# Performance work log

Measured on AMD Instinct MI355X. Metric: run time of the kernel, lower is better.

Reference implementation:

```python
import jax, jax.numpy as jnp
import numpy as np

H = 128  # hidden_dim
F = 64   # node_feat_dim


def setup_inputs() -> dict:
    key = jax.random.key(0)
    ks = jax.random.split(key, 24)
    N, E, NR, NT = 50000, 400000, 20000, 20000
    inp = {
        "mol_x": jax.random.normal(ks[0], (N, F), jnp.float32),
        "pos": jax.random.normal(ks[1], (N, 3), jnp.float32),
        "reaction_x": jax.random.normal(ks[2], (NR, F), jnp.float32),
        "target_x": jax.random.normal(ks[3], (NT, F), jnp.float32),
        "edge_index": jax.random.randint(ks[4], (2, E), 0, N, jnp.int32),
    }
    def lin(k, fan_in, fan_out):
        s = 1.0 / np.sqrt(fan_in)
        kw, kb = jax.random.split(k)
        W = jax.random.uniform(kw, (fan_in, fan_out), jnp.float32, -s, s)
        b = jax.random.uniform(kb, (fan_out,), jnp.float32, -s, s)
        return W, b
    inp["W_node"], inp["b_node"] = lin(ks[5], F, H)
    inp["W_att1"], inp["b_att1"] = lin(ks[6], 2 * H + 3, H)
    inp["W_att2"], inp["b_att2"] = lin(ks[7], H, 1)
    inp["W_upd"], inp["b_upd"] = lin(ks[8], H, H)
    inp["Wy1"], inp["by1"] = lin(ks[9], H, 64)
    inp["Wy2"], inp["by2"] = lin(ks[10], 64, 1)
    inp["Wa1"], inp["ba1"] = lin(ks[11], H, 64)
    inp["Wa2"], inp["ba2"] = lin(ks[12], 64, 1)
    return inp


def reference(mol_x, pos, reaction_x, target_x, edge_index,
              W_node, b_node, W_att1, b_att1, W_att2, b_att2,
              W_upd, b_upd, Wy1, by1, Wy2, by2, Wa1, ba1, Wa2, ba2):
    N = mol_x.shape[0]
    # node encoder
    h = mol_x @ W_node + b_node                      # [N, H]
    src, dst = edge_index[0], edge_index[1]          # PyG: x_j = source, x_i = target
    x_j = h[src]                                      # [E, H]
    x_i = h[dst]                                      # [E, H]
    dist = pos[dst] - pos[src]                        # [E, 3]
    cat = jnp.concatenate([x_i, x_j, dist], axis=1)   # [E, 2H+3]
    s = jax.nn.relu(cat @ W_att1 + b_att1) @ W_att2 + b_att2  # [E, 1]
    att = jax.nn.softmax(s, axis=0)                   # global softmax over edges (dim=0)
    msg = x_j * att                                   # [E, H]
    aggr = jax.ops.segment_sum(msg, dst, num_segments=N)  # scatter-add -> [N, H]
    mol_feats = aggr @ W_upd + b_upd                  # [N, H]
    # heads on reaction / target graphs
    rh = reaction_x @ W_node + b_node
    th = target_x @ W_node + b_node
    pred_yield = (jax.nn.relu(rh @ Wy1 + by1) @ Wy2 + by2).squeeze(-1)
    pred_activity = (jax.nn.relu(th @ Wa1 + ba1) @ Wa2 + ba2).squeeze(-1)
    return pred_yield, pred_activity, mol_feats
```

## Files before the change

### kernel.cpp

```cpp
#include <hip/hip_runtime.h>
#include <hip/hip_bf16.h>

typedef unsigned short ushort_t;
typedef __attribute__((ext_vector_type(8))) short s16x8;
typedef __attribute__((ext_vector_type(4))) float f32x4;

__device__ inline unsigned short f2bf(float x) {
    unsigned u = __float_as_uint(x);
    return (unsigned short)((u + 0x7FFFu + ((u >> 16) & 1u)) >> 16);
}
__device__ inline float bflo(unsigned u) { return __uint_as_float(u << 16); }
__device__ inline float bfhi(unsigned u) { return __uint_as_float(u & 0xffff0000u); }

__device__ inline void pack_one(const float* __restrict__ W, int K, int N,
                                ushort_t* __restrict__ dst, int g) {
    int KT = K / 32;
    int nt = g / (KT * 64);
    int rem = g % (KT * 64);
    int kt = rem / 64, lane = rem % 64;
    int n = nt * 16 + (lane & 15);
    int kbase = kt * 32 + ((lane >> 4) << 3);
    ushort_t tmp[8];
#pragma unroll
    for (int j = 0; j < 8; ++j) tmp[j] = f2bf(W[(size_t)(kbase + j) * N + n]);
    uint4 pk;
    pk.x = tmp[0] | ((unsigned)tmp[1] << 16);
    pk.y = tmp[2] | ((unsigned)tmp[3] << 16);
    pk.z = tmp[4] | ((unsigned)tmp[5] << 16);
    pk.w = tmp[6] | ((unsigned)tmp[7] << 16);
    *(uint4*)&dst[(size_t)g * 8] = pk;
}

__global__ void convert_w(const float* __restrict__ Wn, const float* __restrict__ W1,
                          const float* __restrict__ Wu, const float* __restrict__ Wy1,
                          const float* __restrict__ Wa1,
                          ushort_t* __restrict__ Wnb, ushort_t* __restrict__ W1tb,
                          ushort_t* __restrict__ W1mb, ushort_t* __restrict__ Wub,
                          ushort_t* __restrict__ Wy1b, ushort_t* __restrict__ Wa1b,
                          int* __restrict__ counts, int N) {
    int t = blockIdx.x * 256 + threadIdx.x;
    if (t < 1024)       pack_one(Wn, 64, 128, Wnb, t);
    else if (t < 3072)  pack_one(W1, 128, 128, W1tb, t - 1024);
    else if (t < 5120)  pack_one(W1 + 128 * 128, 128, 128, W1mb, t - 3072);
    else if (t < 7168)  pack_one(Wu, 128, 128, Wub, t - 5120);
    else if (t < 8192)  pack_one(Wy1, 128, 64, Wy1b, t - 7168);
    else if (t < 9216)  pack_one(Wa1, 128, 64, Wa1b, t - 8192);
    if (t < N) counts[t] = 0;
}

__global__ void encode_pq(const float* __restrict__ x, const ushort_t* __restrict__ Wnb,
                          const float* __restrict__ bn, const ushort_t* __restrict__ W1tb,
                          const ushort_t* __restrict__ W1mb, const float* __restrict__ b1,
                          ushort_t* __restrict__ hb, ushort_t* __restrict__ P,
                          ushort_t* __restrict__ Q, const int* __restrict__ dst,
                          int* __restrict__ counts, int nrows, int E) {
    __shared__ ushort_t ldsH[4 * 16 * 136];
    int t = threadIdx.x;
    for (int e = blockIdx.x * 256 + t; e < E; e += gridDim.x * 256)
        atomicAdd(&counts[dst[e]], 1);
    int w = t >> 6, lane = t & 63;
    int c = lane & 15, q = lane >> 4;
    int r0 = blockIdx.x * 64 + w * 16;
    int rowA = r0 + c; if (rowA >= nrows) rowA = nrows - 1;
    ushort_t* myH = &ldsH[w * 16 * 136];

    s16x8 xa[2];
#pragma unroll
    for (int kt = 0; kt < 2; ++kt) {
        const float* xp = &x[(size_t)rowA * 64 + kt * 32 + q * 8];
        float4 v0 = *(const float4*)xp;
        float4 v1 = *(const float4*)(xp + 4);
        s16x8 a;
        a[0] = (short)f2bf(v0.x); a[1] = (short)f2bf(v0.y);
        a[2] = (short)f2bf(v0.z); a[3] = (short)f2bf(v0.w);
        a[4] = (short)f2bf(v1.x); a[5] = (short)f2bf(v1.y);
        a[6] = (short)f2bf(v1.z); a[7] = (short)f2bf(v1.w);
        xa[kt] = a;
    }
#pragma unroll
    for (int nt = 0; nt < 8; ++nt) {
        f32x4 acc = {0.f, 0.f, 0.f, 0.f};
#pragma unroll
        for (int kt = 0; kt < 2; ++kt) {
            s16x8 b = *(const s16x8*)&Wnb[((nt * 2 + kt) * 64 + lane) * 8];
            acc = __builtin_amdgcn_mfma_f32_16x16x32_bf16(xa[kt], b, acc, 0, 0, 0);
        }
        float bi = bn[nt * 16 + c];
#pragma unroll
        for (int r = 0; r < 4; ++r) {
            int row = r0 + q * 4 + r;
            ushort_t hv = f2bf(acc[r] + bi);
            myH[(q * 4 + r) * 136 + nt * 16 + c] = hv;
            if (row < nrows) hb[(size_t)row * 128 + nt * 16 + c] = hv;
        }
    }
    __syncthreads();
    s16x8 ha[4];
#pragma unroll
    for (int kt = 0; kt < 4; ++kt)
        ha[kt] = *(const s16x8*)&myH[c * 136 + kt * 32 + q * 8];
#pragma unroll
    for (int nt = 0; nt < 8; ++nt) {
        f32x4 pa = {0.f, 0.f, 0.f, 0.f}, qa = pa;
#pragma unroll
        for (int kt = 0; kt < 4; ++kt) {
            s16x8 bp = *(const s16x8*)&W1tb[((nt * 4 + kt) * 64 + lane) * 8];
            s16x8 bq = *(const s16x8*)&W1mb[((nt * 4 + kt) * 64 + lane) * 8];
            pa = __builtin_amdgcn_mfma_f32_16x16x32_bf16(ha[kt], bp, pa, 0, 0, 0);
            qa = __builtin_amdgcn_mfma_f32_16x16x32_bf16(ha[kt], bq, qa, 0, 0, 0);
        }
        float bi = b1[nt * 16 + c];
#pragma unroll
        for (int r = 0; r < 4; ++r) {
            int row = r0 + q * 4 + r;
            if (row < nrows) {
                P[(size_t)row * 128 + nt * 16 + c] = f2bf(pa[r] + bi);
                Q[(size_t)row * 128 + nt * 16 + c] = f2bf(qa[r]);
            }
        }
    }
}

__global__ void scan1(const int* __restrict__ counts, int* __restrict__ offs,
                      int* __restrict__ partials, int N) {
    __shared__ int sm[256];
    int i = blockIdx.x * 256 + threadIdx.x;
    int v = (i < N) ? counts[i] : 0;
    sm[threadIdx.x] = v; __syncthreads();
    for (int off = 1; off < 256; off <<= 1) {
        int add = (threadIdx.x >= off) ? sm[threadIdx.x - off] : 0;
        __syncthreads();
        sm[threadIdx.x] += add;
        __syncthreads();
    }
    if (i < N) offs[i] = sm[threadIdx.x] - v;
    if (threadIdx.x == 255) partials[blockIdx.x] = sm[255];
}

__global__ void scan_add(int* __restrict__ offs, int* __restrict__ cursor,
                         const int* __restrict__ partials, int nb, int N) {
    __shared__ int sm[256];
    int t = threadIdx.x;
    sm[t] = (t < nb && t < blockIdx.x) ? partials[t] : 0;
    __syncthreads();
    for (int off = 128; off > 0; off >>= 1) {
        if (t < off) sm[t] += sm[t + off];
        __syncthreads();
    }
    int basev = sm[0];
    int i = blockIdx.x * 256 + t;
    if (i < N) {
        int v = offs[i] + basev;
        offs[i] = v;
        cursor[i] = v;
    }
}

__global__ __launch_bounds__(256, 4)
void edge_score(const ushort_t* __restrict__ P, const ushort_t* __restrict__ Q,
                const float* __restrict__ pos, const int* __restrict__ src,
                const int* __restrict__ dst, const float* __restrict__ W1b,
                const float* __restrict__ W2, const float* __restrict__ b2,
                int* __restrict__ cursor, int2* __restrict__ csr,
                float* __restrict__ redm, float* __restrict__ rede, int E) {
    __shared__ float wsh[512];
    __shared__ float smm[4], sme[4];
    int t = threadIdx.x;
    for (int i = t; i < 384; i += 256) wsh[i] = W1b[i];
    if (t < 128) wsh[384 + t] = W2[t];
    __syncthreads();
    int w = t >> 6, lane = t & 63;
    int g = lane >> 4, c = lane & 15;
    float w0[8], w1[8], w2[8], wv[8];
#pragma unroll
    for (int j = 0; j < 8; ++j) {
        w0[j] = wsh[c * 8 + j];
        w1[j] = wsh[128 + c * 8 + j];
        w2[j] = wsh[256 + c * 8 + j];
        wv[j] = wsh[384 + c * 8 + j];
    }
    float b2v = b2[0];
    int base = blockIdx.x * 128 + w * 32;
    float m = -1e30f, ev = 0.f;
#pragma unroll
    for (int ch = 0; ch < 2; ++ch) {
        int sa[4], da[4];
        int p[4] = {0, 0, 0, 0};
        float d0[4], d1[4], d2[4];
        uint4 pr[4], qr[4];
#pragma unroll
        for (int it = 0; it < 4; ++it) {
            int e = base + ch * 16 + it * 4 + g;
            int ee = (e < E) ? e : (E - 1);
            sa[it] = src[ee];
            da[it] = dst[ee];
        }
#pragma unroll
        for (int it = 0; it < 4; ++it) {
            pr[it] = *(const uint4*)&P[(size_t)da[it] * 128 + c * 8];
            qr[it] = *(const uint4*)&Q[(size_t)sa[it] * 128 + c * 8];
        }
#pragma unroll
        for (int it = 0; it < 4; ++it) {
            d0[it] = pos[da[it] * 3]     - pos[sa[it] * 3];
            d1[it] = pos[da[it] * 3 + 1] - pos[sa[it] * 3 + 1];
            d2[it] = pos[da[it] * 3 + 2] - pos[sa[it] * 3 + 2];
        }
#pragma unroll
        for (int it = 0; it < 4; ++it) {
            int e = base + ch * 16 + it * 4 + g;
            if (c == 0 && e < E) p[it] = atomicAdd(&cursor[da[it]], 1);
        }
#pragma unroll
        for (int it = 0; it < 4; ++it) {
            unsigned pw[4] = {pr[it].x, pr[it].y, pr[it].z, pr[it].w};
            unsigned qw[4] = {qr[it].x, qr[it].y, qr[it].z, qr[it].w};
            float v = 0.f;
#pragma unroll
            for (int jj = 0; jj < 4; ++jj) {
                float pe = bflo(pw[jj]) + bflo(qw[jj])
                         + d0[it] * w0[2 * jj] + d1[it] * w1[2 * jj] + d2[it] * w2[2 * jj];
                float po = bfhi(pw[jj]) + bfhi(qw[jj])
                         + d0[it] * w0[2 * jj + 1] + d1[it] * w1[2 * jj + 1] + d2[it] * w2[2 * jj + 1];
                v += fmaxf(pe, 0.f) * wv[2 * jj] + fmaxf(po, 0.f) * wv[2 * jj + 1];
            }
#pragma unroll
            for (int off = 1; off < 16; off <<= 1) v += __shfl_xor(v, off, 64);
            int e = base + ch * 16 + it * 4 + g;
            if (c == 0 && e < E) {
                float sv = v + b2v;
                csr[p[it]] = make_int2(sa[it], __float_as_int(sv));
                float nm = fmaxf(m, sv);
                ev = ev * __expf(m - nm) + __expf(sv - nm);
                m = nm;
            }
        }
    }
#pragma unroll
    for (int off = 1; off < 64; off <<= 1) {
        float m2 = __shfl_xor(m, off, 64);
        float e2 = __shfl_xor(ev, off, 64);
        float M = fmaxf(m, m2);
        ev = ev * __expf(m - M) + e2 * __expf(m2 - M);
        m = M;
    }
    if (lane == 0) { smm[w] = m; sme[w] = ev; }
    __syncthreads();
    if (t == 0) {
        float m01 = fmaxf(smm[0], smm[1]), m23 = fmaxf(smm[2], smm[3]);
        float M = fmaxf(m01, m23);
        float z = sme[0] * __expf(smm[0] - M) + sme[1] * __expf(smm[1] - M)
                + sme[2] * __expf(smm[2] - M) + sme[3] * __expf(smm[3] - M);
        redm[blockIdx.x] = M;
        rede[blockIdx.x] = z;
    }
}

__global__ void gather_head(const ushort_t* __restrict__ hb, const int2* __restrict__ csr,
                            const int* __restrict__ offs, const int* __restrict__ deg,
                            const float* __restrict__ redm, const float* __restrict__ rede,
                            int nbE,
                            const ushort_t* __restrict__ Wub, const float* __restrict__ bu,
                            float* __restrict__ molf, int N, int nbG,
                            const float* __restrict__ rx, const float* __restrict__ tx,
                            const ushort_t* __restrict__ Wnb, const float* __restrict__ bn,
                            const ushort_t* __restrict__ Wy1b, const float* __restrict__ by1,
                            const float* __restrict__ Wy2, const float* __restrict__ by2,
                            const ushort_t* __restrict__ Wa1b, const float* __restrict__ ba1,
                            const float* __restrict__ Wa2, const float* __restrict__ ba2,
                            float* __restrict__ out, int nb1, int NR, int NT) {
    int t = threadIdx.x;
    int w = t >> 6, lane = t & 63;
    int c = lane & 15, q = lane >> 4;

    if (blockIdx.x < nbG) {
        __shared__ ushort_t ldsA[16 * 136];
        __shared__ float smm[256], sme[256];
        float m = -1e30f, z = 0.f;
        for (int i = t; i < nbE; i += 256) {
            float m2 = redm[i], z2 = rede[i];
            float M = fmaxf(m, m2);
            z = z * __expf(m - M) + z2 * __expf(m2 - M);
            m = M;
        }
        smm[t] = m; sme[t] = z; __syncthreads();
        for (int off = 128; off > 0; off >>= 1) {
            if (t < off) {
                float m1 = smm[t], m2 = smm[t + off];
                float e1 = sme[t], e2 = sme[t + off];
                float M = fmaxf(m1, m2);
                smm[t] = M;
                sme[t] = e1 * __expf(m1 - M) + e2 * __expf(m2 - M);
            }
            __syncthreads();
        }
        float gm = smm[0], inv = 1.f / sme[0];
        __syncthreads();

        int g = lane >> 4;
        int r0 = blockIdx.x * 16;
#pragma unroll
        for (int i = 0; i < 4; ++i) {
            int node = r0 + w * 4 + i;
            float a[8] = {0.f, 0.f, 0.f, 0.f, 0.f, 0.f, 0.f, 0.f};
            if (node < N) {
                int start = offs[node], d = deg[node];
                int k = g;
                for (; k + 4 < d; k += 8) {
                    int2 v0 = csr[start + k];
                    int2 v1 = csr[start + k + 4];
                    uint4 h0 = *(const uint4*)&hb[(size_t)v0.x * 128 + c * 8];
                    uint4 h1 = *(const uint4*)&hb[(size_t)v1.x * 128 + c * 8];
                    float at0 = __expf(__int_as_float(v0.y) - gm) * inv;
                    float at1 = __expf(__int_as_float(v1.y) - gm) * inv;
                    a[0] += bflo(h0.x) * at0; a[1] += bfhi(h0.x) * at0;
                    a[2] += bflo(h0.y) * at0; a[3] += bfhi(h0.y) * at0;
                    a[4] += bflo(h0.z) * at0; a[5] += bfhi(h0.z) * at0;
                    a[6] += bflo(h0.w) * at0; a[7] += bfhi(h0.w) * at0;
                    a[0] += bflo(h1.x) * at1; a[1] += bfhi(h1.x) * at1;
                    a[2] += bflo(h1.y) * at1; a[3] += bfhi(h1.y) * at1;
                    a[4] += bflo(h1.z) * at1; a[5] += bfhi(h1.z) * at1;
                    a[6] += bflo(h1.w) * at1; a[7] += bfhi(h1.w) * at1;
                }
                if (k < d) {
                    int2 v0 = csr[start + k];
                    uint4 h0 = *(const uint4*)&hb[(size_t)v0.x * 128 + c * 8];
                    float at0 = __expf(__int_as_float(v0.y) - gm) * inv;
                    a[0] += bflo(h0.x) * at0; a[1] += bfhi(h0.x) * at0;
                    a[2] += bflo(h0.y) * at0; a[3] += bfhi(h0.y) * at0;
                    a[4] += bflo(h0.z) * at0; a[5] += bfhi(h0.z) * at0;
                    a[6] += bflo(h0.w) * at0; a[7] += bfhi(h0.w) * at0;
                }
            }
#pragma unroll
            for (int j = 0; j < 8; ++j) {
                a[j] += __shfl_xor(a[j], 16, 64);
                a[j] += __shfl_xor(a[j], 32, 64);
            }
            if (g == 0) {
                uint4 pk;
                pk.x = f2bf(a[0]) | ((unsigned)f2bf(a[1]) << 16);
                pk.y = f2bf(a[2]) | ((unsigned)f2bf(a[3]) << 16);
                pk.z = f2bf(a[4]) | ((unsigned)f2bf(a[5]) << 16);
                pk.w = f2bf(a[6]) | ((unsigned)f2bf(a[7]) << 16);
                *(uint4*)&ldsA[(w * 4 + i) * 136 + c * 8] = pk;
            }
        }
        __syncthreads();
        int ntA = w, ntB = w + 4;
        f32x4 acc0 = {0.f, 0.f, 0.f, 0.f}, acc1 = acc0;
#pragma unroll
        for (int kt = 0; kt < 4; ++kt) {
            s16x8 av = *(const s16x8*)&ldsA[c * 136 + kt * 32 + q * 8];
            s16x8 b0 = *(const s16x8*)&Wub[((ntA * 4 + kt) * 64 + lane) * 8];
            s16x8 b1 = *(const s16x8*)&Wub[((ntB * 4 + kt) * 64 + lane) * 8];
            acc0 = __builtin_amdgcn_mfma_f32_16x16x32_bf16(av, b0, acc0, 0, 0, 0);
            acc1 = __builtin_amdgcn_mfma_f32_16x16x32_bf16(av, b1, acc1, 0, 0, 0);
        }
        float bi0 = bu[ntA * 16 + c], bi1 = bu[ntB * 16 + c];
#pragma unroll
        for (int r = 0; r < 4; ++r) {
            int row = r0 + q * 4 + r;
            if (row < N) {
                molf[(size_t)row * 128 + ntA * 16 + c] = acc0[r] + bi0;
                molf[(size_t)row * 128 + ntB * 16 + c] = acc1[r] + bi1;
            }
        }
    } else {
        __shared__ ushort_t ldsX[16 * 72];
        __shared__ ushort_t ldsB[16 * 136];
        __shared__ float part[64];
        int blk = blockIdx.x - nbG;
        const float* x; const ushort_t* W1b; const float* b1; const float* W2; const float* b2;
        float* o; int r0, nrows;
        if (blk < nb1) { x = rx; W1b = Wy1b; b1 = by1; W2 = Wy2; b2 = by2; o = out; r0 = blk * 16; nrows = NR; }
        else { x = tx; W1b = Wa1b; b1 = ba1; W2 = Wa2; b2 = ba2; o = out + NR; r0 = (blk - nb1) * 16; nrows = NT; }
        {
            int row = t >> 4, c4 = (t & 15) * 4;
            float4 v = *(const float4*)&x[(size_t)(r0 + row) * 64 + c4];
            uint2 pk;
            pk.x = f2bf(v.x) | ((unsigned)f2bf(v.y) << 16);
            pk.y = f2bf(v.z) | ((unsigned)f2bf(v.w) << 16);
            *(uint2*)&ldsX[row * 72 + c4] = pk;
        }
        __syncthreads();
        {
            int ntA = w, ntB = w + 4;
            f32x4 acc0 = {0.f, 0.f, 0.f, 0.f}, acc1 = acc0;
#pragma unroll
            for (int kt = 0; kt < 2; ++kt) {
                s16x8 a = *(const s16x8*)&ldsX[c * 72 + kt * 32 + q * 8];
                s16x8 b0 = *(const s16x8*)&Wnb[((ntA * 2 + kt) * 64 + lane) * 8];
                s16x8 b1v = *(const s16x8*)&Wnb[((ntB * 2 + kt) * 64 + lane) * 8];
                acc0 = __builtin_amdgcn_mfma_f32_16x16x32_bf16(a, b0, acc0, 0, 0, 0);
                acc1 = __builtin_amdgcn_mfma_f32_16x16x32_bf16(a, b1v, acc1, 0, 0, 0);
            }
            float bi0 = bn[ntA * 16 + c], bi1 = bn[ntB * 16 + c];
#pragma unroll
            for (int r = 0; r < 4; ++r) {
                int row = q * 4 + r;
                ldsB[row * 136 + ntA * 16 + c] = f2bf(acc0[r] + bi0);
                ldsB[row * 136 + ntB * 16 + c] = f2bf(acc1[r] + bi1);
            }
        }
        __syncthreads();
        {
            f32x4 acc = {0.f, 0.f, 0.f, 0.f};
#pragma unroll
            for (int kt = 0; kt < 4; ++kt) {
                s16x8 a = *(const s16x8*)&ldsB[c * 136 + kt * 32 + q * 8];
                s16x8 b0 = *(const s16x8*)&W1b[((w * 4 + kt) * 64 + lane) * 8];
                acc = __builtin_amdgcn_mfma_f32_16x16x32_bf16(a, b0, acc, 0, 0, 0);
            }
            float bi = b1[w * 16 + c], w2v = W2[w * 16 + c];
#pragma unroll
            for (int r = 0; r < 4; ++r) {
                float u = fmaxf(acc[r] + bi, 0.f) * w2v;
#pragma unroll
                for (int mm = 1; mm < 16; mm <<= 1) u += __shfl_xor(u, mm, 64);
                if (c == 0) part[w * 16 + q * 4 + r] = u;
            }
        }
        __syncthreads();
        if (t < 16) {
            int row = r0 + t;
            if (row < nrows)
                o[row] = part[t] + part[16 + t] + part[32 + t] + part[48 + t] + b2[0];
        }
    }
}

extern "C" void kernel_launch(void* const* d_in, const int* in_sizes, int n_in,
                              void* d_out, int out_size, void* d_ws, size_t ws_size,
                              hipStream_t stream) {
    const float* mol_x      = (const float*)d_in[0];
    const float* pos        = (const float*)d_in[1];
    const float* reaction_x = (const float*)d_in[2];
    const float* target_x   = (const float*)d_in[3];
    const int*   ei         = (const int*)d_in[4];
    const float* W_node = (const float*)d_in[5];
    const float* b_node = (const float*)d_in[6];
    const float* W_att1 = (const float*)d_in[7];
    const float* b_att1 = (const float*)d_in[8];
    const float* W_att2 = (const float*)d_in[9];
    const float* b_att2 = (const float*)d_in[10];
    const float* W_upd  = (const float*)d_in[11];
    const float* b_upd  = (const float*)d_in[12];
    const float* Wy1 = (const float*)d_in[13];
    const float* by1 = (const float*)d_in[14];
    const float* Wy2 = (const float*)d_in[15];
    const float* by2 = (const float*)d_in[16];
    const float* Wa1 = (const float*)d_in[17];
    const float* ba1 = (const float*)d_in[18];
    const float* Wa2 = (const float*)d_in[19];
    const float* ba2 = (const float*)d_in[20];

    int N  = in_sizes[0] / 64;
    int E  = in_sizes[4] / 2;
    int NR = in_sizes[2] / 64;
    int NT = in_sizes[3] / 64;

    float* out = (float*)d_out;

    int nbE = (E + 127) / 128;
    int nbG = (N + 15) / 16;
    int nbH = (NR + NT) / 16;

    char* wp = (char*)d_ws;
    ushort_t* hb = (ushort_t*)wp;  wp += (size_t)N * 128 * 2;
    ushort_t* Qb = (ushort_t*)wp;  wp += (size_t)N * 128 * 2;
    float* redm  = (float*)wp;     wp += (size_t)nbE * 4;
    float* rede  = (float*)wp;     wp += (size_t)nbE * 4;
    int* counts  = (int*)wp;       wp += (size_t)N * 4;
    int* offs    = (int*)wp;       wp += (size_t)N * 4;
    int* cursor  = (int*)wp;       wp += (size_t)N * 4;
    int* partials= (int*)wp;       wp += 256 * 4;
    int2* csr    = (int2*)wp;      wp += (size_t)E * 8;
    ushort_t* Wnb  = (ushort_t*)wp; wp += 8192 * 2;
    ushort_t* W1tb = (ushort_t*)wp; wp += 16384 * 2;
    ushort_t* W1mb = (ushort_t*)wp; wp += 16384 * 2;
    ushort_t* Wub  = (ushort_t*)wp; wp += 16384 * 2;
    ushort_t* Wy1b = (ushort_t*)wp; wp += 8192 * 2;
    ushort_t* Wa1b = (ushort_t*)wp; wp += 8192 * 2;
    ushort_t* Pb = (ushort_t*)(out + NR + NT);
    float* molf  = out + NR + NT;

    const int* srcp = ei;
    const int* dstp = ei + E;
    int nbN = (N + 255) / 256;

    convert_w<<<nbN, 256, 0, stream>>>(W_node, W_att1, W_upd, Wy1, Wa1,
                                       Wnb, W1tb, W1mb, Wub, Wy1b, Wa1b, counts, N);
    encode_pq<<<(N + 63) / 64, 256, 0, stream>>>(mol_x, Wnb, b_node, W1tb, W1mb, b_att1,
                                                 hb, Pb, Qb, dstp, counts, N, E);
    scan1<<<nbN, 256, 0, stream>>>(counts, offs, partials, N);
    scan_add<<<nbN, 256, 0, stream>>>(offs, cursor, partials, nbN, N);
    edge_score<<<nbE, 256, 0, stream>>>(Pb, Qb, pos, srcp, dstp,
                                        W_att1 + 256 * 128, W_att2, b_att2,
                                        cursor, csr, redm, rede, E);
    gather_head<<<nbG + nbH, 256, 0, stream>>>(hb, csr, offs, counts, redm, rede, nbE,
                                               Wub, b_upd, molf, N, nbG,
                                               reaction_x, target_x, Wnb, b_node,
                                               Wy1b, by1, Wy2, by2, Wa1b, ba1, Wa2, ba2,
                                               out, NR / 16, NR, NT);
}
```

Before: 234.9 us.

## Scatter edges into CSR first, score in dst-sorted order, hoist softmax reduce

Adds a separate scatter kernel that places (src,dst) pairs into CSR order with atomics, so edge_score walks edges sorted by destination and reads P rows with locality instead of doing atomics inline. The scores overwrite CSR slots in place. The global softmax max/sum reduction moves out of every gather block into a single-block kernel, removing redundant per-block work. This costs two extra launches and an extra pass over the edge list.

Measured after the change: 236.0 us. No clear change (+0.5%).

```diff
diff --git a/kernel.cpp b/kernel.cpp
--- a/kernel.cpp
+++ b/kernel.cpp
@@ -156,12 +156,21 @@
     }
 }
 
+__global__ void scatter_edges(const int* __restrict__ src, const int* __restrict__ dst,
+                              int* __restrict__ cursor, int2* __restrict__ csr, int E) {
+    int e = blockIdx.x * 256 + threadIdx.x;
+    if (e < E) {
+        int s = src[e], d = dst[e];
+        int p = atomicAdd(&cursor[d], 1);
+        csr[p] = make_int2(s, d);
+    }
+}
+
 __global__ __launch_bounds__(256, 4)
 void edge_score(const ushort_t* __restrict__ P, const ushort_t* __restrict__ Q,
-                const float* __restrict__ pos, const int* __restrict__ src,
-                const int* __restrict__ dst, const float* __restrict__ W1b,
+                const float* __restrict__ pos, const float* __restrict__ W1b,
                 const float* __restrict__ W2, const float* __restrict__ b2,
-                int* __restrict__ cursor, int2* __restrict__ csr,
+                int2* __restrict__ csr,
                 float* __restrict__ redm, float* __restrict__ rede, int E) {
     __shared__ float wsh[512];
     __shared__ float smm[4], sme[4];
@@ -185,31 +194,26 @@
 #pragma unroll
     for (int ch = 0; ch < 2; ++ch) {
         int sa[4], da[4];
-        int p[4] = {0, 0, 0, 0};
         float d0[4], d1[4], d2[4];
         uint4 pr[4], qr[4];
 #pragma unroll
         for (int it = 0; it < 4; ++it) {
-            int e = base + ch * 16 + it * 4 + g;
-            int ee = (e < E) ? e : (E - 1);
-            sa[it] = src[ee];
-            da[it] = dst[ee];
-        }
-#pragma unroll
-        for (int it = 0; it < 4; ++it) {
+            int p = base + ch * 16 + it * 4 + g;
+            int pp = (p < E) ? p : (E - 1);
+            int2 v = csr[pp];
+            sa[it] = v.x; da[it] = v.y;
+        }
+#pragma unroll
+        for (int it = 0; it < 4; ++it)
+            qr[it] = *(const uint4*)&Q[(size_t)sa[it] * 128 + c * 8];
+#pragma unroll
+        for (int it = 0; it < 4; ++it)
             pr[it] = *(const uint4*)&P[(size_t)da[it] * 128 + c * 8];
-            qr[it] = *(const uint4*)&Q[(size_t)sa[it] * 128 + c * 8];
-        }
 #pragma unroll
         for (int it = 0; it < 4; ++it) {
             d0[it] = pos[da[it] * 3]     - pos[sa[it] * 3];
             d1[it] = pos[da[it] * 3 + 1] - pos[sa[it] * 3 + 1];
             d2[it] = pos[da[it] * 3 + 2] - pos[sa[it] * 3 + 2];
-        }
-#pragma unroll
-        for (int it = 0; it < 4; ++it) {
-            int e = base + ch * 16 + it * 4 + g;
-            if (c == 0 && e < E) p[it] = atomicAdd(&cursor[da[it]], 1);
         }
 #pragma unroll
         for (int it = 0; it < 4; ++it) {
@@ -226,10 +230,10 @@
             }
 #pragma unroll
             for (int off = 1; off < 16; off <<= 1) v += __shfl_xor(v, off, 64);
-            int e = base + ch * 16 + it * 4 + g;
-            if (c == 0 && e < E) {
+            int p = base + ch * 16 + it * 4 + g;
+            if (c == 0 && p < E) {
                 float sv = v + b2v;
-                csr[p[it]] = make_int2(sa[it], __float_as_int(sv));
+                csr[p] = make_int2(sa[it], __float_as_int(sv));
                 float nm = fmaxf(m, sv);
                 ev = ev * __expf(m - nm) + __expf(sv - nm);
                 m = nm;
@@ -256,10 +260,35 @@
     }
 }
 
+__global__ void reduce_partials(const float* __restrict__ redm,
+                                const float* __restrict__ rede,
+                                float* __restrict__ gmz, int nbE) {
+    __shared__ float smm[256], sme[256];
+    int t = threadIdx.x;
+    float m = -1e30f, z = 0.f;
+    for (int i = t; i < nbE; i += 256) {
+        float m2 = redm[i], z2 = rede[i];
+        float M = fmaxf(m, m2);
+        z = z * __expf(m - M) + z2 * __expf(m2 - M);
+        m = M;
+    }
+    smm[t] = m; sme[t] = z; __syncthreads();
+    for (int off = 128; off > 0; off >>= 1) {
+        if (t < off) {
+            float m1 = smm[t], m2 = smm[t + off];
+            float e1 = sme[t], e2 = sme[t + off];
+            float M = fmaxf(m1, m2);
+            smm[t] = M;
+            sme[t] = e1 * __expf(m1 - M) + e2 * __expf(m2 - M);
+        }
+        __syncthreads();
+    }
+    if (t == 0) { gmz[0] = smm[0]; gmz[1] = 1.f / sme[0]; }
+}
+
 __global__ void gather_head(const ushort_t* __restrict__ hb, const int2* __restrict__ csr,
                             const int* __restrict__ offs, const int* __restrict__ deg,
-                            const float* __restrict__ redm, const float* __restrict__ rede,
-                            int nbE,
+                            const float* __restrict__ gmz,
                             const ushort_t* __restrict__ Wub, const float* __restrict__ bu,
                             float* __restrict__ molf, int N, int nbG,
                             const float* __restrict__ rx, const float* __restrict__ tx,
@@ -275,27 +304,7 @@
 
     if (blockIdx.x < nbG) {
         __shared__ ushort_t ldsA[16 * 136];
-        __shared__ float smm[256], sme[256];
-        float m = -1e30f, z = 0.f;
-        for (int i = t; i < nbE; i += 256) {
-            float m2 = redm[i], z2 = rede[i];
-            float M = fmaxf(m, m2);
-            z = z * __expf(m - M) + z2 * __expf(m2 - M);
-            m = M;
-        }
-        smm[t] = m; sme[t] = z; __syncthreads();
-        for (int off = 128; off > 0; off >>= 1) {
-            if (t < off) {
-                float m1 = smm[t], m2 = smm[t + off];
-                float e1 = sme[t], e2 = sme[t + off];
-                float M = fmaxf(m1, m2);
-                smm[t] = M;
-                sme[t] = e1 * __expf(m1 - M) + e2 * __expf(m2 - M);
-            }
-            __syncthreads();
-        }
-        float gm = smm[0], inv = 1.f / sme[0];
-        __syncthreads();
+        float gm = gmz[0], inv = gmz[1];
 
         int g = lane >> 4;
         int r0 = blockIdx.x * 16;
@@ -471,6 +480,7 @@
     ushort_t* Qb = (ushort_t*)wp;  wp += (size_t)N * 128 * 2;
     float* redm  = (float*)wp;     wp += (size_t)nbE * 4;
     float* rede  = (float*)wp;     wp += (size_t)nbE * 4;
+    float* gmz   = (float*)wp;     wp += 2 * 4;
     int* counts  = (int*)wp;       wp += (size_t)N * 4;
     int* offs    = (int*)wp;       wp += (size_t)N * 4;
     int* cursor  = (int*)wp;       wp += (size_t)N * 4;
@@ -488,6 +498,7 @@
     const int* srcp = ei;
     const int* dstp = ei + E;
     int nbN = (N + 255) / 256;
+    int nbS = (E + 255) / 256;
 
     convert_w<<<nbN, 256, 0, stream>>>(W_node, W_att1, W_upd, Wy1, Wa1,
                                        Wnb, W1tb, W1mb, Wub, Wy1b, Wa1b, counts, N);
@@ -495,10 +506,12 @@
                                                  hb, Pb, Qb, dstp, counts, N, E);
     scan1<<<nbN, 256, 0, stream>>>(counts, offs, partials, N);
     scan_add<<<nbN, 256, 0, stream>>>(offs, cursor, partials, nbN, N);
-    edge_score<<<nbE, 256, 0, stream>>>(Pb, Qb, pos, srcp, dstp,
+    scatter_edges<<<nbS, 256, 0, stream>>>(srcp, dstp, cursor, csr, E);
+    edge_score<<<nbE, 256, 0, stream>>>(Pb, Qb, pos,
                                         W_att1 + 256 * 128, W_att2, b_att2,
-                                        cursor, csr, redm, rede, E);
-    gather_head<<<nbG + nbH, 256, 0, stream>>>(hb, csr, offs, counts, redm, rede, nbE,
+                                        csr, redm, rede, E);
+    reduce_partials<<<1, 256, 0, stream>>>(redm, rede, gmz, nbE);
+    gather_head<<<nbG + nbH, 256, 0, stream>>>(hb, csr, offs, counts, gmz,
                                                Wub, b_upd, molf, N, nbG,
                                                reaction_x, target_x, Wnb, b_node,
                                                Wy1b, by1, Wy2, by2, Wa1b, ba1, Wa2, ba2,
```
